# Kernel tuning notes

Hardware: AMD Instinct MI355X
Metric: run time of the kernel (lower is better)

Reference implementation:

```python
import jax, jax.numpy as jnp
import numpy as np
import math

NHEAD = 8
OUT = 64
EF = 64
IN = 256
NTYPES = 5
NH = 50000
NT = 100000
E = 800000
NEG_SLOPE = 0.2

def _uniform(key, shape, fan):
    # matches reset(): uniform(-stdv, stdv), stdv = sqrt(6/(fan_in+fan_out)) over last two dims
    stdv = math.sqrt(6.0 / (shape[-2] + shape[-1]))
    return jax.random.uniform(key, shape, jnp.float32, -stdv, stdv)

def setup_inputs() -> dict:
    key = jax.random.key(0)
    ks = jax.random.split(key, 12)
    head_feature = jax.random.normal(ks[0], (NH, IN), jnp.float32)
    tail_feature = jax.random.normal(ks[1], (NT, IN), jnp.float32)
    head_ind = jax.random.randint(ks[2], (E,), 0, NH)
    tail_ind = jax.random.randint(ks[3], (E,), 0, NT)
    tmp_edge = jax.random.randint(ks[4], (E,), 0, NTYPES)
    edge_emb = _uniform(ks[5], (NTYPES, EF), None)
    W = _uniform(ks[6], (IN, OUT * NHEAD), None)
    W_e = _uniform(ks[7], (EF, EF * NHEAD), None)
    a_l = _uniform(ks[8], (1, NHEAD, OUT), None)
    a_r = _uniform(ks[9], (1, NHEAD, OUT), None)
    a_e = _uniform(ks[10], (1, NHEAD, EF), None)
    return {"head_feature": head_feature, "tail_feature": tail_feature,
            "head_ind": head_ind, "tail_ind": tail_ind, "tmp_edge": tmp_edge,
            "edge_emb": edge_emb, "W": W, "W_e": W_e,
            "a_l": a_l, "a_r": a_r, "a_e": a_e}

def reference(head_feature, tail_feature, head_ind, tail_ind, tmp_edge,
              edge_emb, W, W_e, a_l, a_r, a_e):
    n_head_nodes = head_feature.shape[0]
    # projections (dropout is identity in eval)
    h_head = (head_feature @ W).reshape(-1, NHEAD, OUT)   # [NH, H, D]
    h_tail = (tail_feature @ W).reshape(-1, NHEAD, OUT)   # [NT, H, D]
    e = (edge_emb @ W_e).reshape(-1, NHEAD, EF)           # [T, H, EF]
    # per-edge attention logits, all heads at once: [E, H]
    h_l = jnp.sum(a_l * h_head, axis=-1)[head_ind]
    h_r = jnp.sum(a_r * h_tail, axis=-1)[tail_ind]
    h_e = jnp.sum(a_e * e, axis=-1)[tmp_edge]
    att = jax.nn.leaky_relu(h_l + h_r + h_e, NEG_SLOPE)
    # sparse (per-destination-row) softmax, vectorized over heads
    seg_max = jax.ops.segment_max(att, head_ind, num_segments=n_head_nodes)
    att = jnp.exp(att - seg_max[head_ind])
    denom = jax.ops.segment_sum(att, head_ind, num_segments=n_head_nodes)
    att = att / denom[head_ind]                           # [E, H]
    # weighted aggregation per head (small fixed loop over heads)
    outs = [jax.ops.segment_sum(att[:, n:n + 1] * h_tail[tail_ind, n, :],
                                head_ind, num_segments=n_head_nodes)
            for n in range(NHEAD)]
    out = jnp.stack(outs, axis=1).reshape(n_head_nodes, -1)  # [NH, H*D]
    return out, att
```

## Files before the change

### kernel.cpp

```cpp
#include <hip/hip_runtime.h>

#define NH 50000
#define NT 100000
#define NE 800000
#define MPAD 100096

typedef __attribute__((ext_vector_type(8))) short bf16x8;
typedef __attribute__((ext_vector_type(4))) float f32x4;
typedef __attribute__((ext_vector_type(8))) unsigned short u16x8;
typedef __attribute__((ext_vector_type(4))) unsigned int u32x4;

__device__ __forceinline__ unsigned short f2bf(float f){
  unsigned int u = __float_as_uint(f);
  u += 0x7FFFu + ((u >> 16) & 1u);
  return (unsigned short)(u >> 16);
}

__device__ __forceinline__ void fma8(float* acc, float w, uint4 pk){
  acc[0] += w*__uint_as_float(pk.x<<16); acc[1] += w*__uint_as_float(pk.x&0xFFFF0000u);
  acc[2] += w*__uint_as_float(pk.y<<16); acc[3] += w*__uint_as_float(pk.y&0xFFFF0000u);
  acc[4] += w*__uint_as_float(pk.z<<16); acc[5] += w*__uint_as_float(pk.z&0xFFFF0000u);
  acc[6] += w*__uint_as_float(pk.w<<16); acc[7] += w*__uint_as_float(pk.w&0xFFFF0000u);
}

__device__ __forceinline__ void gl2lds16(const unsigned short* g, unsigned short* l){
  __builtin_amdgcn_global_load_lds(
      (const __attribute__((address_space(1))) void*)g,
      (__attribute__((address_space(3))) void*)l, 16, 0, 0);
}

__global__ __launch_bounds__(256) void k_fuse1(
      const float* __restrict__ tail_f, unsigned short* __restrict__ A_bf,
      const int* __restrict__ head_ind, int* __restrict__ cnt,
      const float* __restrict__ W, unsigned short* __restrict__ Wt,
      const float* __restrict__ W_e, const float* __restrict__ edge_emb,
      const float* __restrict__ a_l, const float* __restrict__ a_r,
      const float* __restrict__ a_e,
      unsigned short* __restrict__ wlr_t, float* __restrict__ h_e){
  __shared__ float s_al[512], s_ar[512], s_ae[512], s_wef[512];
  int b = blockIdx.x, t = threadIdx.x;
  if (b < 12500){
    size_t g = (size_t)b*256 + t;
    const float* src = tail_f + g*8;
    float4 v0 = *(const float4*)(src);
    float4 v1 = *(const float4*)(src + 4);
    u16x8 s;
    s[0]=f2bf(v0.x); s[1]=f2bf(v0.y); s[2]=f2bf(v0.z); s[3]=f2bf(v0.w);
    s[4]=f2bf(v1.x); s[5]=f2bf(v1.y); s[6]=f2bf(v1.z); s[7]=f2bf(v1.w);
    *(u16x8*)(A_bf + g*8) = s;
  } else if (b < 15625){
    int e = (b-12500)*256 + t;
    atomicAdd(&cnt[head_ind[e]], 1);
  } else if (b < 16137){
    int n = b - 15625, k = t;
    Wt[n*256+k] = f2bf(W[k*512+n]);
  } else {
    for (int i=t;i<512;i+=256){ s_al[i]=a_l[i]; s_ar[i]=a_r[i]; s_ae[i]=a_e[i]; }
    __syncthreads();
    { int k = t;
      for (int h=0;h<8;h++){
        float accl=0.f, accr=0.f;
        for (int d=0; d<64; d++){
          float w = W[k*512 + h*64 + d];
          accl += w*s_al[h*64+d];
          accr += w*s_ar[h*64+d];
        }
        wlr_t[h*256 + k]     = f2bf(accl);
        wlr_t[(8+h)*256 + k] = f2bf(accr);
      }
    }
    if (t<64){
      for (int h=0;h<8;h++){
        float acc=0.f;
        for (int f=0; f<64; f++) acc += W_e[t*512 + h*64 + f]*s_ae[h*64+f];
        s_wef[t*8+h]=acc;
      }
    }
    __syncthreads();
    if (t<40){
      int ty=t>>3, h=t&7;
      float acc=0.f;
      for (int k2=0;k2<64;k2++) acc += edge_emb[ty*64+k2]*s_wef[k2*8+h];
      h_e[t]=acc;
    }
  }
}

__device__ __forceinline__ void gemm3_body(unsigned short* smem, int bid,
      const unsigned short* __restrict__ A_bf, const unsigned short* __restrict__ Wt,
      const float* __restrict__ a_r_g, unsigned short* __restrict__ Cout,
      float* __restrict__ h_r){
  unsigned short* Asb[2] = { smem, smem + 8192 };
  int t = threadIdx.x;
  int wave = t>>6, lane = t&63;
  int lr = lane & 15, lq = lane >> 4;

  int wg  = (bid & 7)*391 + (bid >> 3);
  int m0 = (wg >> 2)*128;
  int n0 = (wg & 3)*128;
  int wm = (wave>>1)*64, wn = (wave&1)*64;

  f32x4 acc[4][4];
#pragma unroll
  for (int mf=0;mf<4;mf++)
#pragma unroll
    for (int nf=0;nf<4;nf++) acc[mf][nf] = (f32x4){0.f,0.f,0.f,0.f};

  bf16x8 bcur[8], bnxt[8];

#define STAGEA(buf, kt) do { \
    _Pragma("unroll") \
    for (int i=0;i<4;i++){ \
      int v = wave*256 + i*64 + lane; \
      int row = v>>3, un = (v&7) ^ (row&7); \
      gl2lds16(A_bf + (size_t)(m0+row)*256 + (kt)*64 + un*8, \
               &Asb[buf][(wave*256 + i*64)*8]); \
    } } while(0)

#define LOADB(kt, dst) do { \
    _Pragma("unroll") \
    for (int ks=0;ks<2;ks++) \
      _Pragma("unroll") \
      for (int nf=0;nf<4;nf++){ \
        int c = wn + nf*16 + lr; \
        (dst)[ks*4+nf] = *(const bf16x8*)(Wt + (size_t)(n0+c)*256 + ((kt)*8+ks*4+lq)*8); \
      } } while(0)

  STAGEA(0, 0);
  LOADB(0, bcur);
  __syncthreads();
  int cur = 0;
  for (int kt=0; kt<4; kt++){
    if (kt < 3){ STAGEA(cur^1, kt+1); LOADB(kt+1, bnxt); }
#pragma unroll
    for (int ks=0;ks<2;ks++){
      bf16x8 af[4];
#pragma unroll
      for (int mf=0;mf<4;mf++){
        int r = wm + mf*16 + lr;
        int u = (ks*4 + lq) ^ (r&7);
        af[mf] = *(const bf16x8*)((const char*)Asb[cur] + r*128 + u*16);
      }
#pragma unroll
      for (int mf=0;mf<4;mf++)
#pragma unroll
        for (int nf=0;nf<4;nf++)
          acc[mf][nf] = __builtin_amdgcn_mfma_f32_16x16x32_bf16(af[mf], bcur[ks*4+nf], acc[mf][nf], 0,0,0);
    }
    __syncthreads();
    if (kt < 3){
      cur ^= 1;
#pragma unroll
      for (int i=0;i<8;i++) bcur[i] = bnxt[i];
    }
  }
#undef STAGEA
#undef LOADB

  {
    int h = (n0 + wn) >> 6;
    float w[4];
#pragma unroll
    for (int nf=0;nf<4;nf++) w[nf] = a_r_g[h*64 + nf*16 + lr];
#pragma unroll
    for (int mf=0;mf<4;mf++)
#pragma unroll
      for (int j=0;j<4;j++){
        float s = acc[mf][0][j]*w[0] + acc[mf][1][j]*w[1]
                + acc[mf][2][j]*w[2] + acc[mf][3][j]*w[3];
        s += __shfl_xor(s, 1); s += __shfl_xor(s, 2);
        s += __shfl_xor(s, 4); s += __shfl_xor(s, 8);
        int gr = m0 + wm + mf*16 + lq*4 + j;
        if (lr == 0 && gr < NT) h_r[(size_t)gr*8 + h] = s;
      }
  }

  unsigned short* Cs = smem;
#pragma unroll
  for (int mf=0;mf<4;mf++)
#pragma unroll
    for (int nf=0;nf<4;nf++)
#pragma unroll
      for (int j=0;j<4;j++){
        int row = wm + mf*16 + lq*4 + j;
        int cb  = (wn + nf*16 + lr)*2;
        *(unsigned short*)((char*)Cs + row*256 + (cb ^ ((row&12)<<3))) = f2bf(acc[mf][nf][j]);
      }
  __syncthreads();
#pragma unroll
  for (int i=0;i<8;i++){
    int v = i*256 + t;
    int row = v>>4, u = v&15;
    u32x4 val = *(const u32x4*)((const char*)Cs + row*256 + ((u*16) ^ ((row&12)<<3)));
    *(u32x4*)(Cout + (size_t)(m0+row)*512 + n0 + u*8) = val;
  }
}

__device__ __forceinline__ void hl_body(unsigned short* As, unsigned short* Bs, int bid,
      const float* __restrict__ head_f, const unsigned short* __restrict__ wlr_t,
      float* __restrict__ h_l){
  int t = threadIdx.x;
  int wave = t>>6, lane = t&63;
  int lr = lane&15, lq = lane>>4;
  long r0 = (long)bid*256;

#pragma unroll
  for (int i=0;i<2;i++){
    int q = i*256 + t;
    int c = q>>5, un = q&31;
    float4 v = *(const float4*)(wlr_t + c*256 + un*8);
    int u = un ^ (c&7);
    *(float4*)((char*)Bs + c*512 + u*16) = v;
  }

  f32x4 acc[4];
#pragma unroll
  for (int mf=0;mf<4;mf++) acc[mf]=(f32x4){0.f,0.f,0.f,0.f};

  for (int kt=0; kt<4; kt++){
    __syncthreads();
#pragma unroll
    for (int i=0;i<16;i++){
      int q = i*256+t;
      int row = q>>4, cg = q&15;
      long gr = r0 + row;
      float4 v = make_float4(0.f,0.f,0.f,0.f);
      if (gr < NH) v = *(const float4*)(head_f + gr*256 + kt*64 + cg*4);
      int u = (cg>>1) ^ (row&7);
      ushort4 sv;
      sv.x=f2bf(v.x); sv.y=f2bf(v.y); sv.z=f2bf(v.z); sv.w=f2bf(v.w);
      *(ushort4*)((char*)As + row*128 + u*16 + (cg&1)*8) = sv;
    }
    __syncthreads();
#pragma unroll
    for (int ks=0;ks<2;ks++){
      int un = kt*8 + ks*4 + lq;
      int cu = un ^ (lr&7);
      bf16x8 bfr = *(const bf16x8*)((const char*)Bs + lr*512 + cu*16);
#pragma unroll
      for (int mf=0;mf<4;mf++){
        int r = wave*64 + mf*16 + lr;
        int u = (ks*4+lq) ^ (r&7);
        bf16x8 afr = *(const bf16x8*)((const char*)As + r*128 + u*16);
        acc[mf] = __builtin_amdgcn_mfma_f32_16x16x32_bf16(afr, bfr, acc[mf], 0,0,0);
      }
    }
  }
#pragma unroll
  for (int mf=0;mf<4;mf++)
#pragma unroll
    for (int j=0;j<4;j++){
      long grow = r0 + wave*64 + mf*16 + lq*4 + j;
      if (grow < NH && lr < 8) h_l[grow*8+lr] = acc[mf][j];
    }
}

__global__ __launch_bounds__(256) void k_fuse2(
      const unsigned short* __restrict__ A_bf, const unsigned short* __restrict__ Wt,
      const float* __restrict__ a_r_g, unsigned short* __restrict__ Cout,
      float* __restrict__ h_r,
      const float* __restrict__ head_f, const unsigned short* __restrict__ wlr_t,
      float* __restrict__ h_l){
  __shared__ __align__(16) unsigned short smem[20480];
  if (blockIdx.x < 3128)
    gemm3_body(smem, blockIdx.x, A_bf, Wt, a_r_g, Cout, h_r);
  else
    hl_body(smem, smem + 16384, blockIdx.x - 3128, head_f, wlr_t, h_l);
}

__global__ void k_scan1(const int* __restrict__ cnt, int* __restrict__ bsum){
  __shared__ int s[256];
  int b=blockIdx.x, t=threadIdx.x, g=b*256+t;
  s[t] = (g<NH)? cnt[g] : 0;
  __syncthreads();
  for (int off=128; off>0; off>>=1){ if (t<off) s[t]+=s[t+off]; __syncthreads(); }
  if (t==0) bsum[b]=s[0];
}
__global__ void k_scan2(int* __restrict__ bsum, int nb){
  __shared__ int s[256];
  int t=threadIdx.x;
  int v = (t<nb)? bsum[t] : 0;
  s[t]=v; __syncthreads();
  for (int off=1; off<256; off<<=1){
    int u = (t>=off)? s[t-off] : 0; __syncthreads();
    s[t]+=u; __syncthreads();
  }
  if (t<nb) bsum[t] = s[t]-v;
}
__global__ void k_scan3(const int* __restrict__ cnt, const int* __restrict__ bsum,
                        int* __restrict__ offs, int* __restrict__ cur){
  __shared__ int s[256];
  int b=blockIdx.x, t=threadIdx.x, g=b*256+t;
  int v=(g<NH)? cnt[g] : 0;
  s[t]=v; __syncthreads();
  for (int off=1; off<256; off<<=1){
    int u=(t>=off)? s[t-off] : 0; __syncthreads();
    s[t]+=u; __syncthreads();
  }
  int excl = s[t]-v + bsum[b];
  if (g<NH){
    offs[g]=excl; cur[g]=excl;
    if (g==NH-1) offs[NH]=excl+v;
  }
}

__global__ void k_logit2(const int* __restrict__ head_ind, const int* __restrict__ tail_ind,
                         const int* __restrict__ tmp_edge,
                         const float* __restrict__ h_l, const float* __restrict__ h_r,
                         const float* __restrict__ h_e,
                         int* __restrict__ cur,
                         float* __restrict__ att_csr,
                         int* __restrict__ edge_of, int* __restrict__ tail_s){
  int g = blockIdx.x*256 + threadIdx.x;
  int e = g>>3, h = g&7, l = threadIdx.x&63;
  int hd = head_ind[e], tl = tail_ind[e], ty = tmp_edge[e];
  float v = h_l[hd*8+h] + h_r[(size_t)tl*8+h] + h_e[ty*8+h];
  v = v > 0.f ? v : 0.2f*v;
  int p = 0;
  if (h==0) p = atomicAdd(&cur[hd], 1);
  p = __shfl(p, l & ~7);
  att_csr[p*8+h] = v;
  if (h==0){ edge_of[p]=e; tail_s[p]=tl; }
}

__global__ __launch_bounds__(256) void k_agg3(const int* __restrict__ offs,
      const int* __restrict__ edge_of, const int* __restrict__ tail_s,
      const float* __restrict__ att_csr,
      const unsigned short* __restrict__ h_tail,
      float* __restrict__ att, float* __restrict__ out){
  int t = threadIdx.x;
  int l = t & 63;
  int i = blockIdx.x*4 + (t>>6);
  int h = l & 7, hq = l >> 3;
  int s0 = offs[i];
  int deg = offs[i+1] - s0;

  float m = -1e30f;
  for (int q = hq; q < deg; q += 8) m = fmaxf(m, __builtin_nontemporal_load(&att_csr[(s0+q)*8 + h]));
  m = fmaxf(m, __shfl_xor(m, 8));
  m = fmaxf(m, __shfl_xor(m, 16));
  m = fmaxf(m, __shfl_xor(m, 32));
  float sum = 0.f;
  for (int q = hq; q < deg; q += 8) sum += __expf(__builtin_nontemporal_load(&att_csr[(s0+q)*8 + h]) - m);
  sum += __shfl_xor(sum, 8); sum += __shfl_xor(sum, 16); sum += __shfl_xor(sum, 32);
  float r = (deg > 0) ? 1.f/sum : 0.f;

  float mh = __shfl(m, hq), rh = __shfl(r, hq);
  bool wlane = (l & 7) == 0;
  float acc[8];
#pragma unroll
  for (int c=0;c<8;c++) acc[c]=0.f;
  int j = 0;
  for (; j+4 <= deg; j += 4){
    int p0=s0+j, p1=p0+1, p2=p0+2, p3=p0+3;
    int t0=__builtin_nontemporal_load(&tail_s[p0]), t1=__builtin_nontemporal_load(&tail_s[p1]);
    int t2=__builtin_nontemporal_load(&tail_s[p2]), t3=__builtin_nontemporal_load(&tail_s[p3]);
    float a0=__builtin_nontemporal_load(&att_csr[p0*8+hq]), a1=__builtin_nontemporal_load(&att_csr[p1*8+hq]);
    float a2=__builtin_nontemporal_load(&att_csr[p2*8+hq]), a3=__builtin_nontemporal_load(&att_csr[p3*8+hq]);
    uint4 r0 = *(const uint4*)(h_tail + (size_t)t0*512 + l*8);
    uint4 r1 = *(const uint4*)(h_tail + (size_t)t1*512 + l*8);
    uint4 r2 = *(const uint4*)(h_tail + (size_t)t2*512 + l*8);
    uint4 r3 = *(const uint4*)(h_tail + (size_t)t3*512 + l*8);
    float w0=__expf(a0-mh)*rh, w1=__expf(a1-mh)*rh;
    float w2=__expf(a2-mh)*rh, w3=__expf(a3-mh)*rh;
    if (wlane){
      __builtin_nontemporal_store(w0, &att[(size_t)__builtin_nontemporal_load(&edge_of[p0])*8 + hq]);
      __builtin_nontemporal_store(w1, &att[(size_t)__builtin_nontemporal_load(&edge_of[p1])*8 + hq]);
      __builtin_nontemporal_store(w2, &att[(size_t)__builtin_nontemporal_load(&edge_of[p2])*8 + hq]);
      __builtin_nontemporal_store(w3, &att[(size_t)__builtin_nontemporal_load(&edge_of[p3])*8 + hq]);
    }
    fma8(acc, w0, r0);
    fma8(acc, w1, r1);
    fma8(acc, w2, r2);
    fma8(acc, w3, r3);
  }
  for (; j < deg; j++){
    int p0 = s0+j;
    int t0 = __builtin_nontemporal_load(&tail_s[p0]);
    float a0 = __builtin_nontemporal_load(&att_csr[p0*8 + hq]);
    uint4 r0 = *(const uint4*)(h_tail + (size_t)t0*512 + l*8);
    float w0 = __expf(a0 - mh) * rh;
    if (wlane) __builtin_nontemporal_store(w0, &att[(size_t)__builtin_nontemporal_load(&edge_of[p0])*8 + hq]);
    fma8(acc, w0, r0);
  }
  float* o = out + (size_t)i*512 + l*8;
  f32x4 v0 = {acc[0],acc[1],acc[2],acc[3]};
  f32x4 v1 = {acc[4],acc[5],acc[6],acc[7]};
  __builtin_nontemporal_store(v0, (f32x4*)o);
  __builtin_nontemporal_store(v1, (f32x4*)(o+4));
}

extern "C" void kernel_launch(void* const* d_in, const int* in_sizes, int n_in,
                              void* d_out, int out_size, void* d_ws, size_t ws_size,
                              hipStream_t stream) {
  const float* head_f   = (const float*)d_in[0];
  const float* tail_f   = (const float*)d_in[1];
  const int*   head_ind = (const int*)d_in[2];
  const int*   tail_ind = (const int*)d_in[3];
  const int*   tmp_edge = (const int*)d_in[4];
  const float* edge_emb = (const float*)d_in[5];
  const float* W        = (const float*)d_in[6];
  const float* W_e      = (const float*)d_in[7];
  const float* a_l      = (const float*)d_in[8];
  const float* a_r      = (const float*)d_in[9];
  const float* a_e      = (const float*)d_in[10];

  float* out = (float*)d_out;
  float* att = out + (size_t)NH*512;
  unsigned short* A_bf = (unsigned short*)d_out;

  char* ws = (char*)d_ws;
  auto alloc = [&](size_t bytes)->char*{ char* p = ws; ws += (bytes+511)&~(size_t)511; return p; };
  unsigned short* Wt    = (unsigned short*)alloc((size_t)512*256*2);
  unsigned short* wlr_t = (unsigned short*)alloc((size_t)16*256*2);
  float* h_e            = (float*)alloc(512);
  float* h_l            = (float*)alloc((size_t)NH*8*4);
  float* h_r            = (float*)alloc((size_t)NT*8*4);
  unsigned short* h_tail= (unsigned short*)alloc((size_t)MPAD*512*2);
  int* cnt              = (int*)alloc((size_t)NH*4);
  int* offs             = (int*)alloc((size_t)(NH+1)*4);
  int* cur              = (int*)alloc((size_t)NH*4);
  int* bsum             = (int*)alloc(1024);
  int* edge_of          = (int*)alloc((size_t)NE*4);
  int* tail_s           = (int*)alloc((size_t)NE*4);
  float* att_csr        = (float*)alloc((size_t)NE*8*4);

  hipMemsetAsync(cnt, 0, (size_t)NH*4, stream);
  k_fuse1<<<16138,256,0,stream>>>(tail_f, A_bf, head_ind, cnt, W, Wt,
                                  W_e, edge_emb, a_l, a_r, a_e, wlr_t, h_e);
  k_fuse2<<<3128+196,256,0,stream>>>(A_bf, Wt, a_r, h_tail, h_r, head_f, wlr_t, h_l);
  k_scan1<<<196,256,0,stream>>>(cnt, bsum);
  k_scan2<<<1,256,0,stream>>>(bsum, 196);
  k_scan3<<<196,256,0,stream>>>(cnt, bsum, offs, cur);
  k_logit2<<<NE*8/256,256,0,stream>>>(head_ind, tail_ind, tmp_edge, h_l, h_r, h_e,
                                      cur, att_csr, edge_of, tail_s);
  k_agg3<<<NH/4,256,0,stream>>>(offs, edge_of, tail_s, att_csr, h_tail, att, out);
}
```

Before: 421.3 us.

## Unroll GEMM K-loop with manual vmcnt waits, drop scan2, use cached loads in agg

The GEMM main loop is fully unrolled over its four K-steps. Each step has its own B register set, uses raw s_barrier plus explicit vmcnt waits instead of __syncthreads, and keeps the next tile's loads in flight while the current one computes. The separate single-block scan2 kernel is removed; each scan3 block now sums the preceding block totals itself, saving one launch at the cost of redundant serial adds. In the aggregation kernel, nontemporal loads of att_csr, tail_s and edge_of become normal cached loads so repeated reads can hit in cache.

```diff
diff --git a/kernel.cpp b/kernel.cpp
--- a/kernel.cpp
+++ b/kernel.cpp
@@ -90,7 +90,8 @@
       const unsigned short* __restrict__ A_bf, const unsigned short* __restrict__ Wt,
       const float* __restrict__ a_r_g, unsigned short* __restrict__ Cout,
       float* __restrict__ h_r){
-  unsigned short* Asb[2] = { smem, smem + 8192 };
+  unsigned short* As0 = smem;
+  unsigned short* As1 = smem + 8192;
   int t = threadIdx.x;
   int wave = t>>6, lane = t&63;
   int lr = lane & 15, lq = lane >> 4;
@@ -106,56 +107,65 @@
 #pragma unroll
     for (int nf=0;nf<4;nf++) acc[mf][nf] = (f32x4){0.f,0.f,0.f,0.f};
 
-  bf16x8 bcur[8], bnxt[8];
-
-#define STAGEA(buf, kt) do { \
+  bf16x8 b0[8], b1[8], b2[8], b3[8];
+
+#define STAGEA(dst, kt) do { \
     _Pragma("unroll") \
     for (int i=0;i<4;i++){ \
       int v = wave*256 + i*64 + lane; \
       int row = v>>3, un = (v&7) ^ (row&7); \
       gl2lds16(A_bf + (size_t)(m0+row)*256 + (kt)*64 + un*8, \
-               &Asb[buf][(wave*256 + i*64)*8]); \
+               &(dst)[(wave*256 + i*64)*8]); \
     } } while(0)
 
-#define LOADB(kt, dst) do { \
+#define LOADB(kt, bb) do { \
     _Pragma("unroll") \
     for (int ks=0;ks<2;ks++) \
       _Pragma("unroll") \
       for (int nf=0;nf<4;nf++){ \
         int c = wn + nf*16 + lr; \
-        (dst)[ks*4+nf] = *(const bf16x8*)(Wt + (size_t)(n0+c)*256 + ((kt)*8+ks*4+lq)*8); \
+        (bb)[ks*4+nf] = *(const bf16x8*)(Wt + (size_t)(n0+c)*256 + ((kt)*8+ks*4+lq)*8); \
       } } while(0)
 
-  STAGEA(0, 0);
-  LOADB(0, bcur);
-  __syncthreads();
-  int cur = 0;
-  for (int kt=0; kt<4; kt++){
-    if (kt < 3){ STAGEA(cur^1, kt+1); LOADB(kt+1, bnxt); }
-#pragma unroll
-    for (int ks=0;ks<2;ks++){
-      bf16x8 af[4];
-#pragma unroll
-      for (int mf=0;mf<4;mf++){
-        int r = wm + mf*16 + lr;
-        int u = (ks*4 + lq) ^ (r&7);
-        af[mf] = *(const bf16x8*)((const char*)Asb[cur] + r*128 + u*16);
-      }
-#pragma unroll
-      for (int mf=0;mf<4;mf++)
-#pragma unroll
-        for (int nf=0;nf<4;nf++)
-          acc[mf][nf] = __builtin_amdgcn_mfma_f32_16x16x32_bf16(af[mf], bcur[ks*4+nf], acc[mf][nf], 0,0,0);
-    }
-    __syncthreads();
-    if (kt < 3){
-      cur ^= 1;
-#pragma unroll
-      for (int i=0;i<8;i++) bcur[i] = bnxt[i];
-    }
-  }
+#define COMPUTE(Asb, bb) do { \
+    _Pragma("unroll") \
+    for (int ks=0;ks<2;ks++){ \
+      bf16x8 af[4]; \
+      _Pragma("unroll") \
+      for (int mf=0;mf<4;mf++){ \
+        int r = wm + mf*16 + lr; \
+        int u = (ks*4 + lq) ^ (r&7); \
+        af[mf] = *(const bf16x8*)((const char*)(Asb) + r*128 + u*16); \
+      } \
+      _Pragma("unroll") \
+      for (int mf=0;mf<4;mf++) \
+        _Pragma("unroll") \
+        for (int nf=0;nf<4;nf++) \
+          acc[mf][nf] = __builtin_amdgcn_mfma_f32_16x16x32_bf16(af[mf], (bb)[ks*4+nf], acc[mf][nf], 0,0,0); \
+    } } while(0)
+
+#define WAITV(N) asm volatile("s_waitcnt vmcnt(" #N ")" ::: "memory")
+#define RBAR() do { __builtin_amdgcn_s_barrier(); __builtin_amdgcn_sched_barrier(0); } while(0)
+
+  STAGEA(As0, 0); LOADB(0, b0);
+  STAGEA(As1, 1); LOADB(1, b1);
+  WAITV(20); RBAR();
+  COMPUTE(As0, b0);
+  RBAR();
+  STAGEA(As0, 2); LOADB(2, b2);
+  WAITV(20); RBAR();
+  COMPUTE(As1, b1);
+  RBAR();
+  STAGEA(As1, 3); LOADB(3, b3);
+  WAITV(20); RBAR();
+  COMPUTE(As0, b2);
+  WAITV(8);  RBAR();
+  COMPUTE(As1, b3);
 #undef STAGEA
 #undef LOADB
+#undef COMPUTE
+#undef WAITV
+#undef RBAR
 
   {
     int h = (n0 + wn) >> 6;
@@ -175,6 +185,7 @@
       }
   }
 
+  __syncthreads();
   unsigned short* Cs = smem;
 #pragma unroll
   for (int mf=0;mf<4;mf++)
@@ -276,28 +287,21 @@
   for (int off=128; off>0; off>>=1){ if (t<off) s[t]+=s[t+off]; __syncthreads(); }
   if (t==0) bsum[b]=s[0];
 }
-__global__ void k_scan2(int* __restrict__ bsum, int nb){
-  __shared__ int s[256];
-  int t=threadIdx.x;
-  int v = (t<nb)? bsum[t] : 0;
-  s[t]=v; __syncthreads();
-  for (int off=1; off<256; off<<=1){
-    int u = (t>=off)? s[t-off] : 0; __syncthreads();
-    s[t]+=u; __syncthreads();
-  }
-  if (t<nb) bsum[t] = s[t]-v;
-}
 __global__ void k_scan3(const int* __restrict__ cnt, const int* __restrict__ bsum,
                         int* __restrict__ offs, int* __restrict__ cur){
   __shared__ int s[256];
+  __shared__ int sb[196];
   int b=blockIdx.x, t=threadIdx.x, g=b*256+t;
+  if (t < 196) sb[t] = bsum[t];
   int v=(g<NH)? cnt[g] : 0;
   s[t]=v; __syncthreads();
   for (int off=1; off<256; off<<=1){
     int u=(t>=off)? s[t-off] : 0; __syncthreads();
     s[t]+=u; __syncthreads();
   }
-  int excl = s[t]-v + bsum[b];
+  int base = 0;
+  for (int j=0;j<b;j++) base += sb[j];
+  int excl = s[t]-v + base;
   if (g<NH){
     offs[g]=excl; cur[g]=excl;
     if (g==NH-1) offs[NH]=excl+v;
@@ -336,12 +340,12 @@
   int deg = offs[i+1] - s0;
 
   float m = -1e30f;
-  for (int q = hq; q < deg; q += 8) m = fmaxf(m, __builtin_nontemporal_load(&att_csr[(s0+q)*8 + h]));
+  for (int q = hq; q < deg; q += 8) m = fmaxf(m, att_csr[(s0+q)*8 + h]);
   m = fmaxf(m, __shfl_xor(m, 8));
   m = fmaxf(m, __shfl_xor(m, 16));
   m = fmaxf(m, __shfl_xor(m, 32));
   float sum = 0.f;
-  for (int q = hq; q < deg; q += 8) sum += __expf(__builtin_nontemporal_load(&att_csr[(s0+q)*8 + h]) - m);
+  for (int q = hq; q < deg; q += 8) sum += __expf(att_csr[(s0+q)*8 + h] - m);
   sum += __shfl_xor(sum, 8); sum += __shfl_xor(sum, 16); sum += __shfl_xor(sum, 32);
   float r = (deg > 0) ? 1.f/sum : 0.f;
 
@@ -353,10 +357,9 @@
   int j = 0;
   for (; j+4 <= deg; j += 4){
     int p0=s0+j, p1=p0+1, p2=p0+2, p3=p0+3;
-    int t0=__builtin_nontemporal_load(&tail_s[p0]), t1=__builtin_nontemporal_load(&tail_s[p1]);
-    int t2=__builtin_nontemporal_load(&tail_s[p2]), t3=__builtin_nontemporal_load(&tail_s[p3]);
-    float a0=__builtin_nontemporal_load(&att_csr[p0*8+hq]), a1=__builtin_nontemporal_load(&att_csr[p1*8+hq]);
-    float a2=__builtin_nontemporal_load(&att_csr[p2*8+hq]), a3=__builtin_nontemporal_load(&att_csr[p3*8+hq]);
+    int t0=tail_s[p0], t1=tail_s[p1], t2=tail_s[p2], t3=tail_s[p3];
+    float a0=att_csr[p0*8+hq], a1=att_csr[p1*8+hq];
+    float a2=att_csr[p2*8+hq], a3=att_csr[p3*8+hq];
     uint4 r0 = *(const uint4*)(h_tail + (size_t)t0*512 + l*8);
     uint4 r1 = *(const uint4*)(h_tail + (size_t)t1*512 + l*8);
     uint4 r2 = *(const uint4*)(h_tail + (size_t)t2*512 + l*8);
@@ -364,10 +367,10 @@
     float w0=__expf(a0-mh)*rh, w1=__expf(a1-mh)*rh;
     float w2=__expf(a2-mh)*rh, w3=__expf(a3-mh)*rh;
     if (wlane){
-      __builtin_nontemporal_store(w0, &att[(size_t)__builtin_nontemporal_load(&edge_of[p0])*8 + hq]);
-      __builtin_nontemporal_store(w1, &att[(size_t)__builtin_nontemporal_load(&edge_of[p1])*8 + hq]);
-      __builtin_nontemporal_store(w2, &att[(size_t)__builtin_nontemporal_load(&edge_of[p2])*8 + hq]);
-      __builtin_nontemporal_store(w3, &att[(size_t)__builtin_nontemporal_load(&edge_of[p3])*8 + hq]);
+      __builtin_nontemporal_store(w0, &att[(size_t)edge_of[p0]*8 + hq]);
+      __builtin_nontemporal_store(w1, &att[(size_t)edge_of[p1]*8 + hq]);
+      __builtin_nontemporal_store(w2, &att[(size_t)edge_of[p2]*8 + hq]);
+      __builtin_nontemporal_store(w3, &att[(size_t)edge_of[p3]*8 + hq]);
     }
     fma8(acc, w0, r0);
     fma8(acc, w1, r1);
@@ -376,11 +379,11 @@
   }
   for (; j < deg; j++){
     int p0 = s0+j;
-    int t0 = __builtin_nontemporal_load(&tail_s[p0]);
-    float a0 = __builtin_nontemporal_load(&att_csr[p0*8 + hq]);
+    int t0 = tail_s[p0];
+    float a0 = att_csr[p0*8 + hq];
     uint4 r0 = *(const uint4*)(h_tail + (size_t)t0*512 + l*8);
     float w0 = __expf(a0 - mh) * rh;
-    if (wlane) __builtin_nontemporal_store(w0, &att[(size_t)__builtin_nontemporal_load(&edge_of[p0])*8 + hq]);
+    if (wlane) __builtin_nontemporal_store(w0, &att[(size_t)edge_of[p0]*8 + hq]);
     fma8(acc, w0, r0);
   }
   float* o = out + (size_t)i*512 + l*8;
@@ -430,7 +433,6 @@
                                   W_e, edge_emb, a_l, a_r, a_e, wlr_t, h_e);
   k_fuse2<<<3128+196,256,0,stream>>>(A_bf, Wt, a_r, h_tail, h_r, head_f, wlr_t, h_l);
   k_scan1<<<196,256,0,stream>>>(cnt, bsum);
-  k_scan2<<<1,256,0,stream>>>(bsum, 196);
   k_scan3<<<196,256,0,stream>>>(cnt, bsum, offs, cur);
   k_logit2<<<NE*8/256,256,0,stream>>>(head_ind, tail_ind, tmp_edge, h_l, h_r, h_e,
                                       cur, att_csr, edge_of, tail_s);
```

Measured after the change: 418.2 us. About the same (-0.7%).
